# Optimization experiments

Measured on AMD Instinct MI355X. Metric: run time of the kernel, lower is better.

## Reference

```python
import jax, jax.numpy as jnp
import numpy as np

N_NODES = 50000
N_EDGES = 1600000
D = 128
LEAKY_SLOPE = 0.01  # torch nn.LeakyReLU default


def setup_inputs() -> dict:
    key = jax.random.key(0)
    ks = jax.random.split(key, 7)
    entity_embed = jax.random.normal(ks[0], (N_NODES, D), dtype=jnp.float32)
    W1 = jax.random.normal(ks[1], (D, D), dtype=jnp.float32) * 0.05
    b1 = jax.random.normal(ks[2], (D,), dtype=jnp.float32) * 0.05
    W2 = jax.random.normal(ks[3], (D, D), dtype=jnp.float32) * 0.05
    b2 = jax.random.normal(ks[4], (D,), dtype=jnp.float32) * 0.05
    src = jax.random.randint(ks[5], (N_EDGES,), 0, N_NODES, dtype=jnp.int32)
    dst = jax.random.randint(ks[6], (N_EDGES,), 0, N_NODES, dtype=jnp.int32)
    return {"entity_embed": entity_embed, "W1": W1, "b1": b1,
            "W2": W2, "b2": b2, "src": src, "dst": dst}


def reference(entity_embed, W1, b1, W2, b2, src, dst):
    # DGL update_all(copy_u('node','side'), sum('side','H')):
    # H[v] = sum over edges (u -> v) of entity_embed[u]
    n = entity_embed.shape[0]
    H = jax.ops.segment_sum(entity_embed[src], dst, num_segments=n)  # [N, D]
    # neighbors branch: LeakyReLU(W_1 @ H)
    neighbors = jax.nn.leaky_relu(H @ W1.T + b1, negative_slope=LEAKY_SLOPE)
    # interactions branch: LeakyReLU(W_2 @ (node * H))
    interactions = jax.nn.leaky_relu((entity_embed * H) @ W2.T + b2,
                                     negative_slope=LEAKY_SLOPE)
    # dropout is identity at inference
    return neighbors + interactions
```

## Files before the change

kernel.cpp:

```cpp
#include <hip/hip_runtime.h>

#define NN 50000
#define DD 128
#define SLOPE 0.01f
#define NB 782
#define BCAP 2560
#define ECH 6144
#define BST 512
#define PB 2
#define OVCAP 8192
#define HP 136

using bf16x8 = __attribute__((ext_vector_type(8))) short;
using f32x4  = __attribute__((ext_vector_type(4))) float;

__device__ inline float bflo(unsigned int w) { return __uint_as_float(w << 16); }
__device__ inline float bfhi(unsigned int w) { return __uint_as_float(w & 0xffff0000u); }
__device__ inline float sbf(short s) {
    return __uint_as_float(((unsigned int)(unsigned short)s) << 16);
}
__device__ inline unsigned int rnebf(float f) {
    unsigned int u = __float_as_uint(f);
    return (u + 0x7fffu + ((u >> 16) & 1u)) >> 16;
}
__device__ inline unsigned int pack2(float lo, float hi) {
    return rnebf(lo) | (rnebf(hi) << 16);
}
__device__ inline uint4 pack8f(const float* f) {
    uint4 o;
    o.x = pack2(f[0], f[1]); o.y = pack2(f[2], f[3]);
    o.z = pack2(f[4], f[5]); o.w = pack2(f[6], f[7]);
    return o;
}
__device__ inline void addrow(float* acc, uint4 r) {
    acc[0] += bflo(r.x); acc[1] += bfhi(r.x);
    acc[2] += bflo(r.y); acc[3] += bfhi(r.y);
    acc[4] += bflo(r.z); acc[5] += bfhi(r.z);
    acc[6] += bflo(r.w); acc[7] += bfhi(r.w);
}

__global__ __launch_bounds__(BST) void convert_bin(
    const float* __restrict__ E, const float* __restrict__ W1,
    const float* __restrict__ W2, const int* __restrict__ src,
    const int* __restrict__ dst, unsigned short* __restrict__ Ebf,
    unsigned short* __restrict__ W1b, unsigned short* __restrict__ W2b,
    int* __restrict__ gtail, unsigned int* __restrict__ stag,
    int* __restrict__ ovf_cnt, int2* __restrict__ ovf,
    int n_edges, int nbin)
{
    const int tid = threadIdx.x;

    if (blockIdx.x >= nbin) {
        const int NE8 = NN * DD / 8;
        const int NW8 = DD * DD / 8;
        int t = (blockIdx.x - nbin) * BST + tid;
        const float* s; unsigned short* d; int idx;
        if (t < NE8)                { s = E;  d = Ebf; idx = t; }
        else if (t < NE8 + NW8)     { s = W1; d = W1b; idx = t - NE8; }
        else if (t < NE8 + 2 * NW8) { s = W2; d = W2b; idx = t - NE8 - NW8; }
        else return;
        float4 a = ((const float4*)s)[(size_t)idx * 2];
        float4 b = ((const float4*)s)[(size_t)idx * 2 + 1];
        uint4 o;
        o.x = pack2(a.x, a.y); o.y = pack2(a.z, a.w);
        o.z = pack2(b.x, b.y); o.w = pack2(b.z, b.w);
        ((uint4*)d)[idx] = o;
        return;
    }

    __shared__ unsigned int srt[ECH];
    __shared__ int cnt[NB], off[NB], pos[NB];
    __shared__ int wsum[BST / 64];

    const int e0 = blockIdx.x * ECH;
    const int m = min(ECH, n_edges - e0);

    for (int b = tid; b < NB; b += BST) cnt[b] = 0;
    __syncthreads();

    for (int i = tid; i < m; i += BST)
        atomicAdd(&cnt[dst[e0 + i] >> 6], 1);
    __syncthreads();

    const int lane = tid & 63, w = tid >> 6;
    int b0 = tid * PB;
    int loc[PB]; int s = 0;
    #pragma unroll
    for (int j = 0; j < PB; ++j) {
        int bb = b0 + j;
        int cv = (bb < NB) ? cnt[bb] : 0;
        loc[j] = s; s += cv;
    }
    int incl = s;
    #pragma unroll
    for (int d = 1; d < 64; d <<= 1) {
        int t2 = __shfl_up(incl, d);
        if (lane >= d) incl += t2;
    }
    if (lane == 63) wsum[w] = incl;
    __syncthreads();
    int wbase = 0;
    for (int w2 = 0; w2 < w; ++w2) wbase += wsum[w2];
    int base = wbase + incl - s;
    #pragma unroll
    for (int j = 0; j < PB; ++j) {
        int bb = b0 + j;
        if (bb < NB) { off[bb] = base + loc[j]; pos[bb] = base + loc[j]; }
    }
    __syncthreads();

    for (int i = tid; i < m; i += BST) {
        int v = dst[e0 + i];
        int u = src[e0 + i];
        int p = atomicAdd(&pos[v >> 6], 1);
        srt[p] = (unsigned int)u | ((unsigned int)(v & 63) << 16);
    }
    __syncthreads();

    for (int bb = tid; bb < NB; bb += BST) {
        int c = cnt[bb];
        if (!c) continue;
        int g = atomicAdd(&gtail[bb], c);
        int s0 = off[bb];
        unsigned int* dstp = stag + (size_t)bb * BCAP;
        for (int k = 0; k < c; ++k) {
            int gp = g + k;
            unsigned int r = srt[s0 + k];
            if (gp < BCAP) {
                dstp[gp] = r;
            } else {
                int oi = atomicAdd(ovf_cnt, 1);
                if (oi < OVCAP)
                    ovf[oi] = make_int2((int)(r & 0xffffu),
                                        bb * 64 + (int)((r >> 16) & 63));
            }
        }
    }
}

__global__ __launch_bounds__(256) void bucket_fused(
    const unsigned short* __restrict__ Ebf, const int* __restrict__ gtail,
    const unsigned int* __restrict__ stag, const int* __restrict__ ovf_cnt,
    const int2* __restrict__ ovf,
    const unsigned short* __restrict__ W1b, const unsigned short* __restrict__ W2b,
    const float* __restrict__ b1, const float* __restrict__ b2,
    float* __restrict__ out)
{
    __shared__ unsigned short sorted[BCAP];
    __shared__ unsigned short Hs[64][HP];
    __shared__ int cnt[64], off[65], pos[64];
    __shared__ int s_novf;

    const int b = blockIdx.x;
    const int tid = threadIdx.x;
    int len = gtail[b]; len = len < BCAP ? len : BCAP;
    const unsigned int* seg = stag + (size_t)b * BCAP;

    if (tid == 0) { int t = *ovf_cnt; s_novf = t < OVCAP ? t : OVCAP; }
    if (tid < 64) cnt[tid] = 0;
    __syncthreads();
    for (int i = tid; i < len; i += 256)
        atomicAdd(&cnt[(seg[i] >> 16) & 63], 1);
    __syncthreads();
    if (tid == 0) {
        int a = 0;
        for (int j = 0; j < 64; ++j) { off[j] = a; pos[j] = a; a += cnt[j]; }
        off[64] = a;
    }
    __syncthreads();
    for (int i = tid; i < len; i += 256) {
        unsigned int r = seg[i];
        int p = atomicAdd(&pos[(r >> 16) & 63], 1);
        sorted[p] = (unsigned short)(r & 0xffffu);
    }
    __syncthreads();
    const int novf = s_novf;

    const int g = tid >> 4;
    const int c = tid & 15;
    const uint4* E4 = (const uint4*)Ebf;
    for (int p4 = 0; p4 < 4; ++p4) {
        int nl = p4 * 16 + g;
        int v = b * 64 + nl;
        if (v >= NN) continue;
        float acc[8] = {};
        int i = off[nl], e1 = off[nl + 1];
        for (; i + 8 <= e1; i += 8) {
            uint4 r0 = E4[(size_t)sorted[i]     * 16 + c];
            uint4 r1 = E4[(size_t)sorted[i + 1] * 16 + c];
            uint4 r2 = E4[(size_t)sorted[i + 2] * 16 + c];
            uint4 r3 = E4[(size_t)sorted[i + 3] * 16 + c];
            uint4 r4 = E4[(size_t)sorted[i + 4] * 16 + c];
            uint4 r5 = E4[(size_t)sorted[i + 5] * 16 + c];
            uint4 r6 = E4[(size_t)sorted[i + 6] * 16 + c];
            uint4 r7 = E4[(size_t)sorted[i + 7] * 16 + c];
            addrow(acc, r0); addrow(acc, r1); addrow(acc, r2); addrow(acc, r3);
            addrow(acc, r4); addrow(acc, r5); addrow(acc, r6); addrow(acc, r7);
        }
        for (; i + 2 <= e1; i += 2) {
            uint4 r0 = E4[(size_t)sorted[i]     * 16 + c];
            uint4 r1 = E4[(size_t)sorted[i + 1] * 16 + c];
            addrow(acc, r0); addrow(acc, r1);
        }
        if (i < e1) addrow(acc, E4[(size_t)sorted[i] * 16 + c]);

        if (novf > 0) {
            for (int k = 0; k < novf; ++k) {
                int2 e = ovf[k];
                if (e.y == v) addrow(acc, E4[(size_t)e.x * 16 + c]);
            }
        }
        *(uint4*)&Hs[nl][c * 8] = pack8f(acc);
    }
    __syncthreads();

    const int wave = tid >> 6;
    const int lane = tid & 63;
    const int v0 = b * 64 + wave * 16;
    if (v0 >= NN) return;
    const int m = lane & 15;
    const int quad = lane >> 4;

    bf16x8 aH[4], aE[4];
    const unsigned short* hrow = &Hs[wave * 16 + m][quad * 8];
    const unsigned short* erow = Ebf + (size_t)(v0 + m) * DD + quad * 8;
    #pragma unroll
    for (int ks = 0; ks < 4; ++ks) {
        bf16x8 h8 = *(const bf16x8*)(hrow + ks * 32);
        bf16x8 e8 = *(const bf16x8*)(erow + ks * 32);
        aH[ks] = h8;
        bf16x8 eh;
        #pragma unroll
        for (int j = 0; j < 8; ++j)
            eh[j] = (short)rnebf(sbf(h8[j]) * sbf(e8[j]));
        aE[ks] = eh;
    }

    #pragma unroll
    for (int jt = 0; jt < 8; ++jt) {
        const int j0 = jt * 16;
        const unsigned short* w1r = W1b + (size_t)(j0 + m) * DD + quad * 8;
        const unsigned short* w2r = W2b + (size_t)(j0 + m) * DD + quad * 8;
        f32x4 acc1 = {0.f, 0.f, 0.f, 0.f}, acc2 = {0.f, 0.f, 0.f, 0.f};
        #pragma unroll
        for (int ks = 0; ks < 4; ++ks) {
            bf16x8 bw1 = *(const bf16x8*)(w1r + ks * 32);
            bf16x8 bw2 = *(const bf16x8*)(w2r + ks * 32);
            acc1 = __builtin_amdgcn_mfma_f32_16x16x32_bf16(aH[ks], bw1, acc1, 0, 0, 0);
            acc2 = __builtin_amdgcn_mfma_f32_16x16x32_bf16(aE[ks], bw2, acc2, 0, 0, 0);
        }
        const float bb1 = b1[j0 + m], bb2 = b2[j0 + m];
        #pragma unroll
        for (int i = 0; i < 4; ++i) {
            int row = v0 + quad * 4 + i;
            if (row < NN) {
                float x1 = acc1[i] + bb1; x1 = x1 > 0.f ? x1 : SLOPE * x1;
                float x2 = acc2[i] + bb2; x2 = x2 > 0.f ? x2 : SLOPE * x2;
                out[(size_t)row * DD + j0 + m] = x1 + x2;
            }
        }
    }
}

__global__ __launch_bounds__(256) void scatter_add(
    const float* __restrict__ E, const int* __restrict__ src,
    const int* __restrict__ dst, float* __restrict__ H, int n_edges)
{
    int t = blockIdx.x * 256 + threadIdx.x;
    int e = t >> 5;
    if (e >= n_edges) return;
    int c = t & 31;
    float4 a = ((const float4*)E)[(size_t)src[e] * 32 + c];
    float* hp = H + (size_t)dst[e] * DD + c * 4;
    atomicAdd(hp + 0, a.x); atomicAdd(hp + 1, a.y);
    atomicAdd(hp + 2, a.z); atomicAdd(hp + 3, a.w);
}

__global__ __launch_bounds__(256) void fused_mlp(
    const float* __restrict__ E, const float* __restrict__ H,
    const float* __restrict__ W1, const float* __restrict__ b1,
    const float* __restrict__ W2, const float* __restrict__ b2,
    float* __restrict__ out)
{
    __shared__ float Hsf[32][DD];
    __shared__ float EHs[32][DD];
    __shared__ float W1s[DD][20];
    __shared__ float W2s[DD][20];
    const int tid = threadIdx.x;
    const int v0 = blockIdx.x * 32;
    const int nvalid = min(32, NN - v0);
    for (int i = 0; i < 4; ++i) {
        int f = tid + 256 * i;
        int n = f >> 5, c = f & 31;
        float4 h = make_float4(0.f, 0.f, 0.f, 0.f);
        float4 eh = h;
        if (n < nvalid) {
            h = ((const float4*)H)[(size_t)(v0 + n) * 32 + c];
            float4 e4 = ((const float4*)E)[(size_t)(v0 + n) * 32 + c];
            eh = make_float4(e4.x * h.x, e4.y * h.y, e4.z * h.z, e4.w * h.w);
        }
        *((float4*)&Hsf[n][c * 4]) = h;
        *((float4*)&EHs[n][c * 4]) = eh;
    }
    const int jg = tid & 63;
    const int n0 = (tid >> 6) * 8;
    float acc1a[8] = {}, acc1b[8] = {}, acc2a[8] = {}, acc2b[8] = {};
    for (int t8 = 0; t8 < 8; ++t8) {
        const int k0 = t8 * 16;
        __syncthreads();
        for (int i = 0; i < 8; ++i) {
            int f = tid + 256 * i;
            int j = f >> 4, kk = f & 15;
            W1s[j][kk] = W1[j * DD + k0 + kk];
            W2s[j][kk] = W2[j * DD + k0 + kk];
        }
        __syncthreads();
        for (int c = 0; c < 4; ++c) {
            float4 w1a = *((const float4*)&W1s[jg][c * 4]);
            float4 w1b = *((const float4*)&W1s[jg + 64][c * 4]);
            float4 w2a = *((const float4*)&W2s[jg][c * 4]);
            float4 w2b = *((const float4*)&W2s[jg + 64][c * 4]);
            const int kk = k0 + c * 4;
            for (int n = 0; n < 8; ++n) {
                float4 h = *((const float4*)&Hsf[n0 + n][kk]);
                float4 eh = *((const float4*)&EHs[n0 + n][kk]);
                acc1a[n] += h.x * w1a.x + h.y * w1a.y + h.z * w1a.z + h.w * w1a.w;
                acc1b[n] += h.x * w1b.x + h.y * w1b.y + h.z * w1b.z + h.w * w1b.w;
                acc2a[n] += eh.x * w2a.x + eh.y * w2a.y + eh.z * w2a.z + eh.w * w2a.w;
                acc2b[n] += eh.x * w2b.x + eh.y * w2b.y + eh.z * w2b.z + eh.w * w2b.w;
            }
        }
    }
    const float b1a = b1[jg], b1b = b1[jg + 64];
    const float b2a = b2[jg], b2b = b2[jg + 64];
    for (int n = 0; n < 8; ++n) {
        if (n0 + n < nvalid) {
            const int v = v0 + n0 + n;
            float x1 = acc1a[n] + b1a; x1 = x1 > 0.f ? x1 : SLOPE * x1;
            float x2 = acc2a[n] + b2a; x2 = x2 > 0.f ? x2 : SLOPE * x2;
            out[(size_t)v * DD + jg] = x1 + x2;
            float y1 = acc1b[n] + b1b; y1 = y1 > 0.f ? y1 : SLOPE * y1;
            float y2 = acc2b[n] + b2b; y2 = y2 > 0.f ? y2 : SLOPE * y2;
            out[(size_t)v * DD + jg + 64] = y1 + y2;
        }
    }
}

extern "C" void kernel_launch(void* const* d_in, const int* in_sizes, int n_in,
                              void* d_out, int out_size, void* d_ws, size_t ws_size,
                              hipStream_t stream)
{
    const float* E  = (const float*)d_in[0];
    const float* W1 = (const float*)d_in[1];
    const float* b1 = (const float*)d_in[2];
    const float* W2 = (const float*)d_in[3];
    const float* b2 = (const float*)d_in[4];
    const int* src  = (const int*)d_in[5];
    const int* dst  = (const int*)d_in[6];
    float* out = (float*)d_out;
    const int n_edges = in_sizes[5];

    char* ws = (char*)d_ws;
    auto al = [](size_t x) { return (x + 255) & ~(size_t)255; };

    const size_t off_tail = 0;
    const size_t off_ovfc = (size_t)NB * 4;
    const size_t off_ovf  = al(off_ovfc + 4);
    const size_t off_stag = al(off_ovf + (size_t)OVCAP * 8);
    const size_t off_Ebf  = al(off_stag + (size_t)NB * BCAP * 4);
    const size_t off_W1b  = al(off_Ebf + (size_t)NN * DD * 2);
    const size_t off_W2b  = al(off_W1b + (size_t)DD * DD * 2);
    const size_t need_bf  = off_W2b + (size_t)DD * DD * 2;

    if (ws_size >= need_bf) {
        int*  gtail   = (int*)(ws + off_tail);
        int*  ovf_cnt = (int*)(ws + off_ovfc);
        int2* ovf     = (int2*)(ws + off_ovf);
        unsigned int*   stag = (unsigned int*)(ws + off_stag);
        unsigned short* Ebf  = (unsigned short*)(ws + off_Ebf);
        unsigned short* W1b  = (unsigned short*)(ws + off_W1b);
        unsigned short* W2b  = (unsigned short*)(ws + off_W2b);

        const int nbin = (n_edges + ECH - 1) / ECH;
        const int ncv  = NN * DD / 8 + 2 * (DD * DD / 8);
        const int ncvb = (ncv + BST - 1) / BST;

        hipMemsetAsync(ws, 0, off_ovf, stream);
        convert_bin<<<nbin + ncvb, BST, 0, stream>>>(
            E, W1, W2, src, dst, Ebf, W1b, W2b,
            gtail, stag, ovf_cnt, ovf, n_edges, nbin);
        bucket_fused<<<NB, 256, 0, stream>>>(
            Ebf, gtail, stag, ovf_cnt, ovf, W1b, W2b, b1, b2, out);
        return;
    }

    const size_t hbytes = (size_t)NN * DD * sizeof(float);
    float* H = (ws_size >= hbytes) ? (float*)ws : out;
    hipMemsetAsync(H, 0, hbytes, stream);
    scatter_add<<<((n_edges * 32) + 255) / 256, 256, 0, stream>>>(
        E, src, dst, H, n_edges);
    fused_mlp<<<(NN + 31) / 32, 256, 0, stream>>>(E, H, W1, b1, W2, b2, out);
}
```

Baseline: 194.0 us.

## Parallelize bin flush across edges and use 512-thread bucket blocks

The binning kernel's flush loop, which used one thread per bucket and copied edges serially, becomes a per-edge parallel scatter. The bucket index is packed into the high bits of each sorted record and global bases are reserved per bucket first, which removes the long serial per-thread loops. The fused bucket kernel moves to 512 threads: gather work is split over 32 node groups and the MFMA output columns are split between pairs of waves. This roughly halves per-thread serial work, at the cost of more shared memory in the binning kernel and possibly lower occupancy.

```diff
diff --git a/kernel.cpp b/kernel.cpp
--- a/kernel.cpp
+++ b/kernel.cpp
@@ -69,7 +69,7 @@
     }
 
     __shared__ unsigned int srt[ECH];
-    __shared__ int cnt[NB], off[NB], pos[NB];
+    __shared__ int cnt[NB], off[NB], pos[NB], gbase[NB];
     __shared__ int wsum[BST / 64];
 
     const int e0 = blockIdx.x * ECH;
@@ -112,33 +112,35 @@
     for (int i = tid; i < m; i += BST) {
         int v = dst[e0 + i];
         int u = src[e0 + i];
-        int p = atomicAdd(&pos[v >> 6], 1);
-        srt[p] = (unsigned int)u | ((unsigned int)(v & 63) << 16);
+        int bb = v >> 6;
+        int p = atomicAdd(&pos[bb], 1);
+        srt[p] = (unsigned int)u | ((unsigned int)(v & 63) << 16)
+               | ((unsigned int)bb << 22);
     }
     __syncthreads();
 
     for (int bb = tid; bb < NB; bb += BST) {
         int c = cnt[bb];
-        if (!c) continue;
-        int g = atomicAdd(&gtail[bb], c);
-        int s0 = off[bb];
-        unsigned int* dstp = stag + (size_t)bb * BCAP;
-        for (int k = 0; k < c; ++k) {
-            int gp = g + k;
-            unsigned int r = srt[s0 + k];
-            if (gp < BCAP) {
-                dstp[gp] = r;
-            } else {
-                int oi = atomicAdd(ovf_cnt, 1);
-                if (oi < OVCAP)
-                    ovf[oi] = make_int2((int)(r & 0xffffu),
-                                        bb * 64 + (int)((r >> 16) & 63));
-            }
-        }
-    }
-}
-
-__global__ __launch_bounds__(256) void bucket_fused(
+        if (c) gbase[bb] = atomicAdd(&gtail[bb], c);
+    }
+    __syncthreads();
+
+    for (int i = tid; i < m; i += BST) {
+        unsigned int r = srt[i];
+        int bb = (int)(r >> 22);
+        int gp = gbase[bb] + (i - off[bb]);
+        if (gp < BCAP) {
+            stag[(size_t)bb * BCAP + gp] = r & 0x3fffffu;
+        } else {
+            int oi = atomicAdd(ovf_cnt, 1);
+            if (oi < OVCAP)
+                ovf[oi] = make_int2((int)(r & 0xffffu),
+                                    bb * 64 + (int)((r >> 16) & 63));
+        }
+    }
+}
+
+__global__ __launch_bounds__(512) void bucket_fused(
     const unsigned short* __restrict__ Ebf, const int* __restrict__ gtail,
     const unsigned int* __restrict__ stag, const int* __restrict__ ovf_cnt,
     const int2* __restrict__ ovf,
@@ -159,7 +161,7 @@
     if (tid == 0) { int t = *ovf_cnt; s_novf = t < OVCAP ? t : OVCAP; }
     if (tid < 64) cnt[tid] = 0;
     __syncthreads();
-    for (int i = tid; i < len; i += 256)
+    for (int i = tid; i < len; i += 512)
         atomicAdd(&cnt[(seg[i] >> 16) & 63], 1);
     __syncthreads();
     if (tid == 0) {
@@ -168,7 +170,7 @@
         off[64] = a;
     }
     __syncthreads();
-    for (int i = tid; i < len; i += 256) {
+    for (int i = tid; i < len; i += 512) {
         unsigned int r = seg[i];
         int p = atomicAdd(&pos[(r >> 16) & 63], 1);
         sorted[p] = (unsigned short)(r & 0xffffu);
@@ -179,8 +181,8 @@
     const int g = tid >> 4;
     const int c = tid & 15;
     const uint4* E4 = (const uint4*)Ebf;
-    for (int p4 = 0; p4 < 4; ++p4) {
-        int nl = p4 * 16 + g;
+    for (int p2 = 0; p2 < 2; ++p2) {
+        int nl = p2 * 32 + g;
         int v = b * 64 + nl;
         if (v >= NN) continue;
         float acc[8] = {};
@@ -216,13 +218,15 @@
 
     const int wave = tid >> 6;
     const int lane = tid & 63;
-    const int v0 = b * 64 + wave * 16;
+    const int rw = wave >> 1;
+    const int ch = wave & 1;
+    const int v0 = b * 64 + rw * 16;
     if (v0 >= NN) return;
     const int m = lane & 15;
     const int quad = lane >> 4;
 
     bf16x8 aH[4], aE[4];
-    const unsigned short* hrow = &Hs[wave * 16 + m][quad * 8];
+    const unsigned short* hrow = &Hs[rw * 16 + m][quad * 8];
     const unsigned short* erow = Ebf + (size_t)(v0 + m) * DD + quad * 8;
     #pragma unroll
     for (int ks = 0; ks < 4; ++ks) {
@@ -237,7 +241,7 @@
     }
 
     #pragma unroll
-    for (int jt = 0; jt < 8; ++jt) {
+    for (int jt = ch * 4; jt < ch * 4 + 4; ++jt) {
         const int j0 = jt * 16;
         const unsigned short* w1r = W1b + (size_t)(j0 + m) * DD + quad * 8;
         const unsigned short* w2r = W2b + (size_t)(j0 + m) * DD + quad * 8;
@@ -389,7 +393,7 @@
         convert_bin<<<nbin + ncvb, BST, 0, stream>>>(
             E, W1, W2, src, dst, Ebf, W1b, W2b,
             gtail, stag, ovf_cnt, ovf, n_edges, nbin);
-        bucket_fused<<<NB, 256, 0, stream>>>(
+        bucket_fused<<<NB, 512, 0, stream>>>(
             Ebf, gtail, stag, ovf_cnt, ovf, W1b, W2b, b1, b2, out);
         return;
     }
```

After: 191.2 us. About the same (-1.4%).
